# Kernel optimization log

Hardware: AMD Instinct MI355X
Metric: run time of the kernel (lower is better)

## Reference

```python
import jax, jax.numpy as jnp
import numpy as np

B, G, C = 16384, 7, 30  # batch, 7x7 grid, 2*5 box params + 20 classes


def setup_inputs() -> dict:
    key = jax.random.key(0)
    k1, k2 = jax.random.split(key)
    pred = jax.random.uniform(k1, (B, G, G, C), dtype=jnp.float32)
    labels = jax.random.uniform(k2, (B, G, G, C), dtype=jnp.float32)
    # channel 0 of labels is the object-presence indicator (==1 where a gt box exists)
    labels = labels.at[..., 0].set((labels[..., 0] > 0.7).astype(jnp.float32))
    return {"pred": pred, "labels": labels}


def _corners(box):
    # box channels: [conf, x, y, w, h]
    x, y, w, h = box[..., 1], box[..., 2], box[..., 3], box[..., 4]
    return x - 0.5 * w, x + 0.5 * w, y - 0.5 * h, y + 0.5 * h  # left,right,top,bottom


def _iou(b1, b2):
    l1, r1, t1, bt1 = _corners(b1)
    l2, r2, t2, bt2 = _corners(b2)
    in_h = jnp.minimum(bt1, bt2) - jnp.maximum(t1, t2)
    in_w = jnp.minimum(r1, r2) - jnp.maximum(l1, l2)
    inter = jnp.where((in_h < 0) | (in_w < 0), 0.0, in_h * in_w)
    area1 = (bt1 - t1) * (r1 - l1)
    area2 = (bt2 - t2) * (r2 - l2)
    return inter / (area1 + area2 - inter)


def reference(pred, labels):
    mask = labels[..., 0]                     # [B,7,7] object indicator (0/1)
    box1 = pred[..., 0:5]
    box2 = pred[..., 5:10]
    gt = labels[..., 0:5]
    iou1 = _iou(box1, gt)
    iou2 = _iou(box2, gt)
    best = iou1 >= iou2                       # responsible box per cell
    sel = jnp.where(best[..., None], box1, box2)
    iou_max = jnp.where(best, iou1, iou2)
    iou_min = jnp.where(best, iou2, iou1)
    center = 5.0 * ((sel[..., 1] - gt[..., 1]) ** 2 + (sel[..., 2] - gt[..., 2]) ** 2)
    wh = 5.0 * ((jnp.sqrt(sel[..., 3]) - jnp.sqrt(gt[..., 3])) ** 2
                + (jnp.sqrt(sel[..., 4]) - jnp.sqrt(gt[..., 4])) ** 2)
    cls = jnp.sum((pred[..., 10:] - labels[..., 10:]) ** 2, axis=-1)

    def msum(x):
        return jnp.sum(x * mask)

    # [center, wh, obj_conf, noobj_conf, classification]
    return jnp.stack([msum(center), msum(wh), msum(iou_max), msum(iou_min), msum(cls)])
```

## Files before the change

### kernel.cpp

```cpp
#include <hip/hip_runtime.h>
#include <stdint.h>

#define NCH   30
#define TPB   128
#define TILE  128
#define TW    (TILE * NCH)
#define TF4   (TW / 4)
#define NBLK  1280

__device__ __forceinline__ float iou_f(float x1, float y1, float w1, float h1,
                                       float x2, float y2, float w2, float h2) {
    float l1 = x1 - 0.5f * w1, r1 = x1 + 0.5f * w1;
    float t1 = y1 - 0.5f * h1, b1 = y1 + 0.5f * h1;
    float l2 = x2 - 0.5f * w2, r2 = x2 + 0.5f * w2;
    float t2 = y2 - 0.5f * h2, b2 = y2 + 0.5f * h2;
    float in_h = fminf(b1, b2) - fmaxf(t1, t2);
    float in_w = fminf(r1, r2) - fmaxf(l1, l2);
    float inter = (in_h < 0.f || in_w < 0.f) ? 0.f : in_h * in_w;
    float a1 = (b1 - t1) * (r1 - l1);
    float a2 = (b2 - t2) * (r2 - l2);
    return inter / (a1 + a2 - inter);
}

__device__ __forceinline__ void cell_loss(const float* __restrict__ pp,
                                          const float* __restrict__ lp,
                                          float& v0, float& v1, float& v2,
                                          float& v3, float& v4) {
    const float2 l01 = *(const float2*)(lp);
    const float mask = l01.x;
    if (mask == 0.f) return;

    const float2 l23 = *(const float2*)(lp + 2);
    const float2 l45 = *(const float2*)(lp + 4);
    const float gx = l01.y, gy = l23.x, gw = l23.y, gh = l45.x;

    const float2 p01 = *(const float2*)(pp);
    const float2 p23 = *(const float2*)(pp + 2);
    const float2 p45 = *(const float2*)(pp + 4);
    const float2 p67 = *(const float2*)(pp + 6);
    const float2 p89 = *(const float2*)(pp + 8);

    const float i1 = iou_f(p01.y, p23.x, p23.y, p45.x, gx, gy, gw, gh);
    const float i2 = iou_f(p67.x, p67.y, p89.x, p89.y, gx, gy, gw, gh);
    const bool best = (i1 >= i2);
    const float sx = best ? p01.y : p67.x;
    const float sy = best ? p23.x : p67.y;
    const float sw = best ? p23.y : p89.x;
    const float sh = best ? p45.x : p89.y;
    const float imax = best ? i1 : i2;
    const float imin = best ? i2 : i1;

    const float center = 5.f * ((sx - gx) * (sx - gx) + (sy - gy) * (sy - gy));
    const float dw = sqrtf(sw) - sqrtf(gw);
    const float dh = sqrtf(sh) - sqrtf(gh);
    const float wh = 5.f * (dw * dw + dh * dh);

    float cls = 0.f;
#pragma unroll
    for (int k = 0; k < 10; ++k) {
        const float2 pd = *(const float2*)(pp + 10 + 2 * k);
        const float2 ld = *(const float2*)(lp + 10 + 2 * k);
        const float dx = pd.x - ld.x;
        const float dy = pd.y - ld.y;
        cls += dx * dx + dy * dy;
    }

    v0 += center * mask;
    v1 += wh * mask;
    v2 += imax * mask;
    v3 += imin * mask;
    v4 += cls * mask;
}

__global__ __launch_bounds__(TPB) void yolo_partial(const float* __restrict__ pred,
                                                    const float* __restrict__ lab,
                                                    float* __restrict__ partial,
                                                    int n_cells) {
    __shared__ float sl[TW];
    __shared__ float sp[TW];
    __shared__ unsigned long long sbits[TPB / 64];
    __shared__ float red[5][TPB / 64];

    const int tid  = threadIdx.x;
    const int wave = tid >> 6;
    const int lane = tid & 63;
    const int bid  = blockIdx.x;
    const int NB   = gridDim.x;
    const int nt   = n_cells / TILE;

    float v0 = 0.f, v1 = 0.f, v2 = 0.f, v3 = 0.f, v4 = 0.f;

    for (int t = bid; t < nt; t += NB) {
        const size_t base = (size_t)t * TW;

#pragma unroll
        for (int i = 0; i < 8; ++i) {
            const int idx = i * TPB + tid;
            if (idx < TF4)
                *(float4*)(sl + (size_t)idx * 4) =
                    *(const float4*)(lab + base + (size_t)idx * 4);
        }
        __syncthreads();

        const float my_mask = sl[tid * NCH];
        const unsigned long long bits = __ballot(my_mask != 0.f);
        if (lane == 0) sbits[wave] = bits;
        __syncthreads();

        const unsigned long long b0 = sbits[0];
        const unsigned long long b1 = sbits[1];

#pragma unroll
        for (int i = 0; i < 8; ++i) {
            const int idx = i * TPB + tid;
            if (idx < TF4) {
                const int f0 = idx * 4;
                const int c0 = f0 / NCH;
                const int c1 = (f0 + 3) / NCH;
                const bool n0 = (c0 < 64) ? ((b0 >> c0) & 1ull) : ((b1 >> (c0 - 64)) & 1ull);
                const bool n1 = (c1 < 64) ? ((b0 >> c1) & 1ull) : ((b1 >> (c1 - 64)) & 1ull);
                if (n0 || n1)
                    *(float4*)(sp + (size_t)idx * 4) =
                        *(const float4*)(pred + base + (size_t)idx * 4);
            }
        }
        __syncthreads();

        cell_loss(sp + tid * NCH, sl + tid * NCH, v0, v1, v2, v3, v4);
        __syncthreads();
    }

    const int rem_start = nt * TILE;
    if (bid == 0 && rem_start < n_cells) {
        for (int c = rem_start + tid; c < n_cells; c += TPB) {
            cell_loss(pred + (size_t)c * NCH, lab + (size_t)c * NCH,
                      v0, v1, v2, v3, v4);
        }
    }

#pragma unroll
    for (int off = 32; off > 0; off >>= 1) {
        v0 += __shfl_down(v0, off);
        v1 += __shfl_down(v1, off);
        v2 += __shfl_down(v2, off);
        v3 += __shfl_down(v3, off);
        v4 += __shfl_down(v4, off);
    }
    if (lane == 0) {
        red[0][wave] = v0;
        red[1][wave] = v1;
        red[2][wave] = v2;
        red[3][wave] = v3;
        red[4][wave] = v4;
    }
    __syncthreads();
    if (tid < 5) {
        float sacc = 0.f;
#pragma unroll
        for (int w = 0; w < TPB / 64; ++w) sacc += red[tid][w];
        partial[(size_t)bid * 5 + tid] = sacc;
    }
}

__global__ __launch_bounds__(256) void final_reduce(const float* __restrict__ partial,
                                                    float* __restrict__ out,
                                                    int n_blocks) {
    __shared__ float red[5][4];
    const int tid = threadIdx.x;
    float v0 = 0.f, v1 = 0.f, v2 = 0.f, v3 = 0.f, v4 = 0.f;
    for (int b = tid; b < n_blocks; b += 256) {
        const float* p = partial + (size_t)b * 5;
        v0 += p[0]; v1 += p[1]; v2 += p[2]; v3 += p[3]; v4 += p[4];
    }
#pragma unroll
    for (int off = 32; off > 0; off >>= 1) {
        v0 += __shfl_down(v0, off);
        v1 += __shfl_down(v1, off);
        v2 += __shfl_down(v2, off);
        v3 += __shfl_down(v3, off);
        v4 += __shfl_down(v4, off);
    }
    const int wave = tid >> 6;
    const int lane = tid & 63;
    if (lane == 0) {
        red[0][wave] = v0;
        red[1][wave] = v1;
        red[2][wave] = v2;
        red[3][wave] = v3;
        red[4][wave] = v4;
    }
    __syncthreads();
    if (tid < 5) {
        float sacc = 0.f;
#pragma unroll
        for (int w = 0; w < 4; ++w) sacc += red[tid][w];
        out[tid] = sacc;
    }
}

extern "C" void kernel_launch(void* const* d_in, const int* in_sizes, int n_in,
                              void* d_out, int out_size, void* d_ws, size_t ws_size,
                              hipStream_t stream) {
    const float* pred = (const float*)d_in[0];
    const float* lab  = (const float*)d_in[1];
    float* out = (float*)d_out;
    float* partial = (float*)d_ws;

    const int n_cells = in_sizes[0] / NCH;

    hipLaunchKernelGGL(yolo_partial, dim3(NBLK), dim3(TPB), 0, stream,
                       pred, lab, partial, n_cells);
    hipLaunchKernelGGL(final_reduce, dim3(1), dim3(256), 0, stream,
                       partial, out, NBLK);
}
```

Baseline: 215.4 us.

## Load pred and labels tiles together in one unmasked pass, dropping ballot gating

Replaces the two-phase load, which read the labels tile, ballotted the object masks, then fetched only the pred chunks needed by masked cells, with one pass that loads both pred and labels for a 64-cell tile into a shared buffer. This removes one barrier and the serial label-then-pred dependency, and issues all global loads up front with 256 threads and more blocks. The cost is reading all of pred, including the roughly 70% of cells with no object that the old code skipped, and only a quarter of the threads compute per tile.

```diff
diff --git a/kernel.cpp b/kernel.cpp
--- a/kernel.cpp
+++ b/kernel.cpp
@@ -2,11 +2,11 @@
 #include <stdint.h>
 
 #define NCH   30
-#define TPB   128
-#define TILE  128
+#define TPB   256
+#define TILE  64
 #define TW    (TILE * NCH)
 #define TF4   (TW / 4)
-#define NBLK  1280
+#define NBLK  2048
 
 __device__ __forceinline__ float iou_f(float x1, float y1, float w1, float h1,
                                        float x2, float y2, float w2, float h2) {
@@ -76,9 +76,7 @@
                                                     const float* __restrict__ lab,
                                                     float* __restrict__ partial,
                                                     int n_cells) {
-    __shared__ float sl[TW];
-    __shared__ float sp[TW];
-    __shared__ unsigned long long sbits[TPB / 64];
+    __shared__ float s[2 * TW];
     __shared__ float red[5][TPB / 64];
 
     const int tid  = threadIdx.x;
@@ -90,43 +88,37 @@
 
     float v0 = 0.f, v1 = 0.f, v2 = 0.f, v3 = 0.f, v4 = 0.f;
 
+    const int i0 = tid, i1 = tid + TPB, i2 = tid + 2 * TPB, i3 = tid + 3 * TPB;
+
     for (int t = bid; t < nt; t += NB) {
-        const size_t base = (size_t)t * TW;
-
-#pragma unroll
-        for (int i = 0; i < 8; ++i) {
-            const int idx = i * TPB + tid;
-            if (idx < TF4)
-                *(float4*)(sl + (size_t)idx * 4) =
-                    *(const float4*)(lab + base + (size_t)idx * 4);
+        const size_t gbase = (size_t)t * TW;
+
+        {
+            const float4* s0 = (const float4*)((i0 < TF4 ? pred + gbase + (size_t)i0 * 4
+                                                         : lab  + gbase + (size_t)(i0 - TF4) * 4));
+            const float4* s1 = (const float4*)((i1 < TF4 ? pred + gbase + (size_t)i1 * 4
+                                                         : lab  + gbase + (size_t)(i1 - TF4) * 4));
+            const float4* s2 = (const float4*)((i2 < TF4 ? pred + gbase + (size_t)i2 * 4
+                                                         : lab  + gbase + (size_t)(i2 - TF4) * 4));
+            float4 r0 = *s0;
+            float4 r1 = *s1;
+            float4 r2 = *s2;
+            float4 r3;
+            if (i3 < 2 * TF4) {
+                const float4* s3 = (const float4*)((i3 < TF4 ? pred + gbase + (size_t)i3 * 4
+                                                             : lab  + gbase + (size_t)(i3 - TF4) * 4));
+                r3 = *s3;
+            }
+            *(float4*)(s + (size_t)i0 * 4) = r0;
+            *(float4*)(s + (size_t)i1 * 4) = r1;
+            *(float4*)(s + (size_t)i2 * 4) = r2;
+            if (i3 < 2 * TF4) *(float4*)(s + (size_t)i3 * 4) = r3;
         }
         __syncthreads();
 
-        const float my_mask = sl[tid * NCH];
-        const unsigned long long bits = __ballot(my_mask != 0.f);
-        if (lane == 0) sbits[wave] = bits;
-        __syncthreads();
-
-        const unsigned long long b0 = sbits[0];
-        const unsigned long long b1 = sbits[1];
-
-#pragma unroll
-        for (int i = 0; i < 8; ++i) {
-            const int idx = i * TPB + tid;
-            if (idx < TF4) {
-                const int f0 = idx * 4;
-                const int c0 = f0 / NCH;
-                const int c1 = (f0 + 3) / NCH;
-                const bool n0 = (c0 < 64) ? ((b0 >> c0) & 1ull) : ((b1 >> (c0 - 64)) & 1ull);
-                const bool n1 = (c1 < 64) ? ((b0 >> c1) & 1ull) : ((b1 >> (c1 - 64)) & 1ull);
-                if (n0 || n1)
-                    *(float4*)(sp + (size_t)idx * 4) =
-                        *(const float4*)(pred + base + (size_t)idx * 4);
-            }
+        if (tid < TILE) {
+            cell_loss(s + tid * NCH, s + TW + tid * NCH, v0, v1, v2, v3, v4);
         }
-        __syncthreads();
-
-        cell_loss(sp + tid * NCH, sl + tid * NCH, v0, v1, v2, v3, v4);
         __syncthreads();
     }
 
```

After: 210.8 us. -2.1%, faster.
